# Kernel optimization log

Measured on AMD Instinct MI355X. Metric: run time of the kernel, lower is better.

Reference implementation:

```python
import jax, jax.numpy as jnp
import numpy as np

KH = KW = 3
K = KH * KW


def _conv_same(x, w, b):
    y = jax.lax.conv_general_dilated(
        x, w, window_strides=(1, 1), padding='SAME',
        dimension_numbers=('NHWC', 'HWIO', 'NHWC'))
    return y + b


def setup_inputs() -> dict:
    key = jax.random.key(0)
    ks = jax.random.split(key, 5)
    B, H, W, C, F = 4, 128, 128, 128, 256
    x = jax.random.normal(ks[0], (B, H, W, C), dtype=jnp.float32)
    offset_w = jax.random.normal(ks[1], (KH, KW, C, 2 * K), dtype=jnp.float32) * 0.02
    offset_b = jnp.zeros((2 * K,), dtype=jnp.float32)
    mod_w = jax.random.normal(ks[2], (KH, KW, C, K), dtype=jnp.float32) * 0.02
    mod_b = jnp.zeros((K,), dtype=jnp.float32)
    kernel = jax.random.normal(ks[3], (KH, KW, C, F), dtype=jnp.float32) * (1.0 / np.sqrt(K * C))
    bias = jnp.zeros((F,), dtype=jnp.float32)
    return {'x': x, 'offset_w': offset_w, 'offset_b': offset_b,
            'mod_w': mod_w, 'mod_b': mod_b, 'kernel': kernel, 'bias': bias}


def _forward(x, offset_w, offset_b, mod_w, mod_b, kernel, bias):
    B, H, W, C = x.shape
    F = kernel.shape[-1]
    offsets = _conv_same(x, offset_w, offset_b)                      # [B,H,W,2K]
    modulation = jax.nn.sigmoid(_conv_same(x, mod_w, mod_b))         # [B,H,W,K]
    offsets = offsets.reshape(B, H, W, K, 2)
    modulation = modulation.reshape(B, H, W, K, 1)

    # Base grid: ONLY relative kernel offsets (faithful to the original, which
    # does not add the per-pixel (y,x) anchor).
    ky, kx = jnp.meshgrid(jnp.arange(-(KH // 2), KH // 2 + 1, dtype=jnp.float32),
                          jnp.arange(-(KW // 2), KW // 2 + 1, dtype=jnp.float32),
                          indexing='ij')
    base = jnp.stack([ky, kx], axis=-1).reshape(1, 1, 1, K, 2)
    grid = base + offsets                                            # [B,H,W,K,2]

    gy = jnp.clip(grid[..., 0], 0.0, H - 1)
    gx = jnp.clip(grid[..., 1], 0.0, W - 1)
    y0 = jnp.floor(gy).astype(jnp.int32)
    x0 = jnp.floor(gx).astype(jnp.int32)
    y1 = jnp.minimum(y0 + 1, H - 1)
    x1 = jnp.minimum(x0 + 1, W - 1)
    wy1 = (gy - y0)[..., None]
    wy0 = 1.0 - wy1
    wx1 = (gx - x0)[..., None]
    wx0 = 1.0 - wx1

    b_idx = jnp.arange(B)[:, None, None, None]
    v00 = x[b_idx, y0, x0]   # [B,H,W,K,C]
    v01 = x[b_idx, y0, x1]
    v10 = x[b_idx, y1, x0]
    v11 = x[b_idx, y1, x1]
    sampled = wy0 * (wx0 * v00 + wx1 * v01) + wy1 * (wx0 * v10 + wx1 * v11)

    sampled = (sampled * modulation).reshape(B, H, W, K * C)
    out = jnp.einsum('bhwf,fo->bhwo', sampled, kernel.reshape(K * C, F)) + bias
    return out


def reference(x, offset_w, offset_b, mod_w, mod_b, kernel, bias):
    return _forward(x, offset_w, offset_b, mod_w, mod_b, kernel, bias)
```

## Files before the change

### kernel.cpp

```cpp
#include <hip/hip_runtime.h>
#include <hip/hip_bf16.h>
#include <math.h>

typedef __attribute__((ext_vector_type(8))) short bf16x8;
typedef __attribute__((ext_vector_type(8))) unsigned short u16x8;
typedef __attribute__((ext_vector_type(4))) float f32x4;
typedef unsigned short ushort_t;


__device__ __forceinline__ ushort_t f2bf(float f) {
    union { float f; unsigned int u; } v; v.f = f;
    unsigned int u = v.u;
    return (ushort_t)((u + 0x7fffu + ((u >> 16) & 1u)) >> 16);
}

__device__ __forceinline__ ushort2 pk_bf16(float a, float b) {
    __hip_bfloat162 h = __float22bfloat162_rn(make_float2(a, b));
    return *(ushort2*)&h;
}

__device__ __forceinline__ float bflo(unsigned v) {
    union { unsigned u; float f; } c; c.u = v << 16; return c.f;
}
__device__ __forceinline__ float bfhi(unsigned v) {
    union { unsigned u; float f; } c; c.u = v & 0xffff0000u; return c.f;
}

__global__ __launch_bounds__(256) void k0_prep(
    const float* __restrict__ x, const float* __restrict__ kern,
    const float* __restrict__ offw, const float* __restrict__ modw,
    ushort_t* __restrict__ xbf, ushort_t* __restrict__ wt2,
    ushort_t* __restrict__ wom2) {
    const int gid = blockIdx.x, t = threadIdx.x;
    if (gid < 8192) {
        const int idx = gid * 256 + t;
        float4 v = ((const float4*)x)[idx];
        ushort4 u;
        u.x = f2bf(v.x); u.y = f2bf(v.y); u.z = f2bf(v.z); u.w = f2bf(v.w);
        ((ushort4*)xbf)[idx] = u;
    } else if (gid < 9344) {
        const int tid = (gid - 8192) * 256 + t;
        const int kpart = tid & 31, n = (tid >> 5) & 255, kcg = tid >> 13;
        const int k = kcg * 32 + kpart;
        wt2[tid] = f2bf(kern[k * 256 + n]);
    } else {
        const int tid = (gid - 9344) * 256 + t;
        const int kpart = tid & 31, n = (tid >> 5) & 31, kcg = tid >> 10;
        const int k = kcg * 32 + kpart;
        float v = 0.f;
        if (n < 18) v = offw[k * 18 + n];
        else if (n < 27) v = modw[k * 9 + (n - 18)];
        wom2[tid] = f2bf(v);
    }
}

#define XSS 72
__global__ __launch_bounds__(256) void k1_offsets(
    const ushort_t* __restrict__ xbf, const ushort_t* __restrict__ wom2,
    const float* __restrict__ offb, const float* __restrict__ modb,
    float4* __restrict__ metaw, int2* __restrict__ metai) {
    __shared__ ushort_t xs[3 * 130 * XSS];
    float* Cs = (float*)xs;
    const int bid = blockIdx.x;
    const int b = bid >> 7, h = bid & 127;
    const int t = threadIdx.x;
    const int lane = t & 63, wv = t >> 6;
    const int ln = lane & 15, quad = lane >> 4;

    f32x4 acc[2][2];
#pragma unroll
    for (int i = 0; i < 2; ++i)
#pragma unroll
        for (int j = 0; j < 2; ++j) acc[i][j] = (f32x4){0.f, 0.f, 0.f, 0.f};

    for (int half = 0; half < 2; ++half) {
        for (int u = t; u < 768; u += 256) {
            const int r = u >> 8, rem = u & 255;
            const int xw = rem >> 1, sub = rem & 1;
            const int y = h + r - 1;
            ushort_t* dst = &xs[(r * 130 + xw + 1) * XSS + sub * 32];
            if ((unsigned)y < 128u) {
                const ushort_t* src = xbf + (((b * 128 + y) * 128 + xw) * 128) + half * 64 + sub * 32;
#pragma unroll
                for (int j = 0; j < 4; ++j)
                    *(int4*)(dst + j * 8) = *(const int4*)(src + j * 8);
            } else {
                const int4 z = make_int4(0, 0, 0, 0);
#pragma unroll
                for (int j = 0; j < 4; ++j) *(int4*)(dst + j * 8) = z;
            }
        }
        if (t < 48) {
            const int r = t >> 4, side = (t >> 3) & 1, j = t & 7;
            *(int4*)&xs[(r * 130 + side * 129) * XSS + j * 8] = make_int4(0, 0, 0, 0);
        }
        __syncthreads();
#pragma unroll
        for (int tap = 0; tap < 9; ++tap) {
            const int ky = tap / 3, kx = tap % 3;
#pragma unroll
            for (int kc = 0; kc < 2; ++kc) {
                const int col = kc * 32 + quad * 8;
                const ushort_t* arow = &xs[(ky * 130 + kx) * XSS + col];
                bf16x8 a0 = *(const bf16x8*)(arow + (wv * 32 + ln) * XSS);
                bf16x8 a1 = *(const bf16x8*)(arow + (wv * 32 + 16 + ln) * XSS);
                const int kcg = tap * 4 + half * 2 + kc;
                const ushort_t* bp = wom2 + kcg * 1024 + quad * 8;
                bf16x8 b0 = *(const bf16x8*)(bp + ln * 32);
                bf16x8 b1 = *(const bf16x8*)(bp + (ln + 16) * 32);
                acc[0][0] = __builtin_amdgcn_mfma_f32_16x16x32_bf16(a0, b0, acc[0][0], 0, 0, 0);
                acc[0][1] = __builtin_amdgcn_mfma_f32_16x16x32_bf16(a0, b1, acc[0][1], 0, 0, 0);
                acc[1][0] = __builtin_amdgcn_mfma_f32_16x16x32_bf16(a1, b0, acc[1][0], 0, 0, 0);
                acc[1][1] = __builtin_amdgcn_mfma_f32_16x16x32_bf16(a1, b1, acc[1][1], 0, 0, 0);
            }
        }
        __syncthreads();
    }
#pragma unroll
    for (int mi = 0; mi < 2; ++mi)
#pragma unroll
        for (int nt = 0; nt < 2; ++nt)
#pragma unroll
            for (int r = 0; r < 4; ++r) {
                const int m = wv * 32 + mi * 16 + quad * 4 + r;
                const int n = nt * 16 + ln;
                if (n < 27) Cs[m * 32 + n] = acc[mi][nt][r];
            }
    __syncthreads();
    const int px = t >> 1;
    const int p = bid * 128 + px;
    for (int tap = (t & 1); tap < 9; tap += 2) {
        const float oy = Cs[px * 32 + 2 * tap] + offb[2 * tap];
        const float ox = Cs[px * 32 + 2 * tap + 1] + offb[2 * tap + 1];
        float md = Cs[px * 32 + 18 + tap] + modb[tap];
        md = 1.f / (1.f + __expf(-md));
        const float gy = fminf(fmaxf((float)(tap / 3 - 1) + oy, 0.f), 127.f);
        const float gx = fminf(fmaxf((float)(tap % 3 - 1) + ox, 0.f), 127.f);
        const float y0f = floorf(gy), x0f = floorf(gx);
        const int y0 = (int)y0f, x0 = (int)x0f;
        const int dy = (y0 < 127) ? 16384 : 0;
        const int dx = (x0 < 127) ? 128 : 0;
        const float wy1 = gy - y0f, wx1 = gx - x0f;
        const float wy0 = 1.f - wy1, wx0 = 1.f - wx1;
        metaw[p * 9 + tap] = make_float4(md * wy0 * wx0, md * wy0 * wx1,
                                         md * wy1 * wx0, md * wy1 * wx1);
        metai[p * 9 + tap] = make_int2((y0 * 128 + x0) * 128, dy + dx);
    }
}

__device__ __forceinline__ u16x8 lerp8(uint4 a, uint4 b, uint4 c, uint4 d, float4 w) {
    const unsigned* pa = (const unsigned*)&a;
    const unsigned* pb = (const unsigned*)&b;
    const unsigned* pc = (const unsigned*)&c;
    const unsigned* pd = (const unsigned*)&d;
    u16x8 r;
#pragma unroll
    for (int j = 0; j < 4; ++j) {
        float sl = w.x * bflo(pa[j]) + w.y * bflo(pb[j]) + w.z * bflo(pc[j]) + w.w * bflo(pd[j]);
        float sh = w.x * bfhi(pa[j]) + w.y * bfhi(pb[j]) + w.z * bfhi(pc[j]) + w.w * bfhi(pd[j]);
        ushort2 pk2 = pk_bf16(sl, sh);
        r[2 * j] = pk2.x; r[2 * j + 1] = pk2.y;
    }
    return r;
}

__device__ __forceinline__ void stage64(ushort_t* __restrict__ dst,
                                        const ushort_t* __restrict__ xb,
                                        int si, int cb, float4 w, int2 mi_) {
    const ushort_t* r00 = xb + mi_.x + cb * 16;
    const ushort_t* r01 = r00 + (mi_.y & 128);
    const ushort_t* r10 = r00 + (mi_.y & 16384);
    const ushort_t* r11 = r00 + mi_.y;
    uint4 u00a = *(const uint4*)r00, u00b = *(const uint4*)(r00 + 8);
    uint4 u01a = *(const uint4*)r01, u01b = *(const uint4*)(r01 + 8);
    uint4 u10a = *(const uint4*)r10, u10b = *(const uint4*)(r10 + 8);
    uint4 u11a = *(const uint4*)r11, u11b = *(const uint4*)(r11 + 8);
    const int sw = si & 15;
    *(u16x8*)&dst[si * 128 + (((cb * 2) ^ sw) << 3)]     = lerp8(u00a, u01a, u10a, u11a, w);
    *(u16x8*)&dst[si * 128 + (((cb * 2 + 1) ^ sw) << 3)] = lerp8(u00b, u01b, u10b, u11b, w);
}

__global__ __launch_bounds__(512, 4) void k2_main(
    const ushort_t* __restrict__ xbf, const ushort_t* __restrict__ wt2,
    const float4* __restrict__ metaw, const int2* __restrict__ metai,
    const float* __restrict__ bias, float* __restrict__ out) {
    __shared__ ushort_t As[2 * 8192];
    const int bid = blockIdx.x;
    const int b = bid >> 8;
    const int t = threadIdx.x;
    const int lane = t & 63, wv = t >> 6;
    const int ln = lane & 15, quad = lane >> 4;
    const int ng = wv;
    const int p0 = bid * 64;

    f32x4 acc[4][2];
#pragma unroll
    for (int i = 0; i < 4; ++i)
#pragma unroll
        for (int j = 0; j < 2; ++j) acc[i][j] = (f32x4){0.f, 0.f, 0.f, 0.f};

    const int si = t >> 3, cb = t & 7;
    const int p = p0 + si;
    const ushort_t* xb = xbf + b * (1 << 21);

    float4 mw0 = metaw[p * 9];
    int2 mi0 = metai[p * 9];
    stage64(As, xb, si, cb, mw0, mi0);
    float4 mwN = metaw[p * 9 + 1];
    int2 miN = metai[p * 9 + 1];
    __syncthreads();

    for (int tap = 0; tap < 9; ++tap) {
        const ushort_t* buf = As + (tap & 1) * 8192;
#pragma unroll
        for (int kc = 0; kc < 4; ++kc) {
            const int chunk = kc * 4 + quad;
            bf16x8 a[4], bb[2];
#pragma unroll
            for (int mi2 = 0; mi2 < 4; ++mi2) {
                const int m = mi2 * 16 + ln;
                a[mi2] = *(const bf16x8*)&buf[m * 128 + ((chunk ^ ln) << 3)];
            }
            const int kcg = tap * 4 + kc;
#pragma unroll
            for (int nj = 0; nj < 2; ++nj) {
                const int n = ng * 32 + nj * 16 + ln;
                bb[nj] = *(const bf16x8*)&wt2[(kcg * 256 + n) * 32 + quad * 8];
            }
#pragma unroll
            for (int mi2 = 0; mi2 < 4; ++mi2)
#pragma unroll
                for (int nj = 0; nj < 2; ++nj)
                    acc[mi2][nj] = __builtin_amdgcn_mfma_f32_16x16x32_bf16(
                        a[mi2], bb[nj], acc[mi2][nj], 0, 0, 0);
        }
        if (tap < 8) {
            float4 mwP; int2 miP;
            if (tap < 7) { mwP = metaw[p * 9 + tap + 2]; miP = metai[p * 9 + tap + 2]; }
            stage64(As + ((tap + 1) & 1) * 8192, xb, si, cb, mwN, miN);
            mwN = mwP; miN = miP;
        }
        __syncthreads();
    }
#pragma unroll
    for (int mi2 = 0; mi2 < 4; ++mi2)
#pragma unroll
        for (int nj = 0; nj < 2; ++nj) {
            const int n = ng * 32 + nj * 16 + ln;
            const float bs = bias[n];
#pragma unroll
            for (int r = 0; r < 4; ++r) {
                const int m = mi2 * 16 + quad * 4 + r;
                out[(p0 + m) * 256 + n] = acc[mi2][nj][r] + bs;
            }
        }
}

extern "C" void kernel_launch(void* const* d_in, const int* in_sizes, int n_in,
                              void* d_out, int out_size, void* d_ws, size_t ws_size,
                              hipStream_t stream) {
    const float* x    = (const float*)d_in[0];
    const float* offw = (const float*)d_in[1];
    const float* offb = (const float*)d_in[2];
    const float* modw = (const float*)d_in[3];
    const float* modb = (const float*)d_in[4];
    const float* kern = (const float*)d_in[5];
    const float* bias = (const float*)d_in[6];
    float* out = (float*)d_out;

    char* ws = (char*)d_ws;
    ushort_t* xbf   = (ushort_t*)(ws);
    ushort_t* wt2   = (ushort_t*)(ws + 16777216);
    ushort_t* wom2  = (ushort_t*)(ws + 17367040);
    float4*   metaw = (float4*)(ws + 17440768);
    int2*     metai = (int2*)(ws + 26877952);

    k0_prep<<<9488, 256, 0, stream>>>(x, kern, offw, modw, xbf, wt2, wom2);
    k1_offsets<<<512, 256, 0, stream>>>(xbf, wom2, offb, modb, metaw, metai);
    k2_main<<<1024, 512, 0, stream>>>(xbf, wt2, metaw, metai, bias, out);
}
```

Measured before the change: 184.9 us.

## Fuse x bf16 conversion into offset-conv kernel so both run concurrently

The large prep kernel is split. A tiny kernel now converts only the offset/modulation weights. The x-to-bf16 and main-weight conversion blocks are appended to the offset-conv launch, so they run alongside the conv blocks instead of before them. The offset-conv blocks read fp32 x directly and convert it to bf16 while staging it in shared memory, which removes their dependency on xbf. This cuts one serialized stage, but the conv blocks now read twice as many bytes, and the two kinds of blocks compete for the same CUs.

```diff
diff --git a/kernel.cpp b/kernel.cpp
--- a/kernel.cpp
+++ b/kernel.cpp
@@ -26,44 +26,52 @@
     union { unsigned u; float f; } c; c.u = v & 0xffff0000u; return c.f;
 }
 
-__global__ __launch_bounds__(256) void k0_prep(
+__global__ __launch_bounds__(256) void kA1_womprep(
+    const float* __restrict__ offw, const float* __restrict__ modw,
+    ushort_t* __restrict__ wom2) {
+    const int tid = blockIdx.x * 256 + threadIdx.x;
+    const int kpart = tid & 31, n = (tid >> 5) & 31, kcg = tid >> 10;
+    const int k = kcg * 32 + kpart;
+    float v = 0.f;
+    if (n < 18) v = offw[k * 18 + n];
+    else if (n < 27) v = modw[k * 9 + (n - 18)];
+    wom2[tid] = f2bf(v);
+}
+
+#define XSS 72
+__global__ __launch_bounds__(256) void kA2_prep(
     const float* __restrict__ x, const float* __restrict__ kern,
-    const float* __restrict__ offw, const float* __restrict__ modw,
+    const ushort_t* __restrict__ wom2,
+    const float* __restrict__ offb, const float* __restrict__ modb,
     ushort_t* __restrict__ xbf, ushort_t* __restrict__ wt2,
-    ushort_t* __restrict__ wom2) {
-    const int gid = blockIdx.x, t = threadIdx.x;
-    if (gid < 8192) {
-        const int idx = gid * 256 + t;
-        float4 v = ((const float4*)x)[idx];
-        ushort4 u;
-        u.x = f2bf(v.x); u.y = f2bf(v.y); u.z = f2bf(v.z); u.w = f2bf(v.w);
-        ((ushort4*)xbf)[idx] = u;
-    } else if (gid < 9344) {
-        const int tid = (gid - 8192) * 256 + t;
-        const int kpart = tid & 31, n = (tid >> 5) & 255, kcg = tid >> 13;
-        const int k = kcg * 32 + kpart;
-        wt2[tid] = f2bf(kern[k * 256 + n]);
-    } else {
-        const int tid = (gid - 9344) * 256 + t;
-        const int kpart = tid & 31, n = (tid >> 5) & 31, kcg = tid >> 10;
-        const int k = kcg * 32 + kpart;
-        float v = 0.f;
-        if (n < 18) v = offw[k * 18 + n];
-        else if (n < 27) v = modw[k * 9 + (n - 18)];
-        wom2[tid] = f2bf(v);
-    }
-}
-
-#define XSS 72
-__global__ __launch_bounds__(256) void k1_offsets(
-    const ushort_t* __restrict__ xbf, const ushort_t* __restrict__ wom2,
-    const float* __restrict__ offb, const float* __restrict__ modb,
     float4* __restrict__ metaw, int2* __restrict__ metai) {
     __shared__ ushort_t xs[3 * 130 * XSS];
+    const int gid = blockIdx.x;
+    const int t = threadIdx.x;
+
+    if (gid >= 512) {
+        const int g2 = gid - 512;
+        if (g2 < 1024) {
+#pragma unroll
+            for (int i = 0; i < 8; ++i) {
+                const int idx = (g2 * 256 + t) + i * (1024 * 256);
+                float4 v = ((const float4*)x)[idx];
+                ushort4 u;
+                u.x = f2bf(v.x); u.y = f2bf(v.y); u.z = f2bf(v.z); u.w = f2bf(v.w);
+                ((ushort4*)xbf)[idx] = u;
+            }
+        } else {
+            const int tid = (g2 - 1024) * 256 + t;
+            const int kpart = tid & 31, n = (tid >> 5) & 255, kcg = tid >> 13;
+            const int k = kcg * 32 + kpart;
+            wt2[tid] = f2bf(kern[k * 256 + n]);
+        }
+        return;
+    }
+
     float* Cs = (float*)xs;
-    const int bid = blockIdx.x;
+    const int bid = gid;
     const int b = bid >> 7, h = bid & 127;
-    const int t = threadIdx.x;
     const int lane = t & 63, wv = t >> 6;
     const int ln = lane & 15, quad = lane >> 4;
 
@@ -80,10 +88,18 @@
             const int y = h + r - 1;
             ushort_t* dst = &xs[(r * 130 + xw + 1) * XSS + sub * 32];
             if ((unsigned)y < 128u) {
-                const ushort_t* src = xbf + (((b * 128 + y) * 128 + xw) * 128) + half * 64 + sub * 32;
-#pragma unroll
-                for (int j = 0; j < 4; ++j)
-                    *(int4*)(dst + j * 8) = *(const int4*)(src + j * 8);
+                const float* src = x + (((b * 128 + y) * 128 + xw) * 128) + half * 64 + sub * 32;
+#pragma unroll
+                for (int j = 0; j < 4; ++j) {
+                    float4 va = *(const float4*)(src + j * 8);
+                    float4 vb = *(const float4*)(src + j * 8 + 4);
+                    u16x8 ov;
+                    ov[0] = f2bf(va.x); ov[1] = f2bf(va.y);
+                    ov[2] = f2bf(va.z); ov[3] = f2bf(va.w);
+                    ov[4] = f2bf(vb.x); ov[5] = f2bf(vb.y);
+                    ov[6] = f2bf(vb.z); ov[7] = f2bf(vb.w);
+                    *(u16x8*)(dst + j * 8) = ov;
+                }
             } else {
                 const int4 z = make_int4(0, 0, 0, 0);
 #pragma unroll
@@ -275,7 +291,7 @@
     float4*   metaw = (float4*)(ws + 17440768);
     int2*     metai = (int2*)(ws + 26877952);
 
-    k0_prep<<<9488, 256, 0, stream>>>(x, kern, offw, modw, xbf, wt2, wom2);
-    k1_offsets<<<512, 256, 0, stream>>>(xbf, wom2, offb, modb, metaw, metai);
+    kA1_womprep<<<144, 256, 0, stream>>>(offw, modw, wom2);
+    kA2_prep<<<2688, 256, 0, stream>>>(x, kern, wom2, offb, modb, xbf, wt2, metaw, metai);
     k2_main<<<1024, 512, 0, stream>>>(xbf, wt2, metaw, metai, bias, out);
 }
```

After: 192.8 us. 4.3% more time.
